# Kernel tuning notes

Hardware: AMD Instinct MI355X
Metric: run time of the kernel (lower is better)

## Reference

```python
import jax, jax.numpy as jnp
import numpy as np

EPS = 1e-7

def squash(t, axis=-1):
    sq = jnp.sum(jnp.square(t), axis=axis, keepdims=True)
    safe_norm = jnp.sqrt(sq + EPS)
    return t * (sq / (1.0 + sq)) / safe_norm


def setup_inputs() -> dict:
    key = jax.random.key(0)
    k1, k2 = jax.random.split(key)
    B, I, Din, N, D = 32, 1024, 32, 64, 32
    x = jax.random.normal(k1, (B, I, Din), dtype=jnp.float32)
    # glorot-ish scale ~ sqrt(2/(Din+D)) = 0.1767; use 0.1
    W = jax.random.normal(k2, (N, I, D, Din), dtype=jnp.float32) * 0.1
    return {"x": x, "W": W, "num_routing": 3}


def _infer(inputs_hat, logits):
    # softmax over the num_capsule axis (axis=1), matching tf.nn.softmax(logits, axis=1)
    route = jax.nn.softmax(logits, axis=1)                      # [B,N,1,I]
    routing = jnp.squeeze(jnp.matmul(route, inputs_hat), -2)    # [B,N,D]
    return squash(routing)


def reference(x, W, num_routing):
    # inputs_hat[b,n,i,d] = sum_k x[b,i,k] * W[n,i,d,k]
    inputs_hat = jnp.einsum('bik,nidk->bnid', x, W)             # [B,N,I,D]
    B, N, I, D = inputs_hat.shape
    ih_stop = jax.lax.stop_gradient(inputs_hat)
    logits = jnp.zeros((B, N, 1, I), dtype=inputs_hat.dtype)
    outputs = None
    for r in range(num_routing):
        if r == num_routing - 1:
            outputs = _infer(inputs_hat, logits)
        else:
            outputs = _infer(ih_stop, logits)
            # distances[b,n,1,i] = <outputs[b,n,:], ih_stop[b,n,i,:]>
            dist = jnp.matmul(outputs[:, :, None, :], jnp.swapaxes(ih_stop, -1, -2))
            logits = logits + dist
    return outputs
```

## Files before the change

### kernel.cpp

```cpp
#include <hip/hip_runtime.h>
#include <stdint.h>

#define II 1024
#define BBc 32
#define NN 64
#define DD 32
#define NDT 2048

typedef _Float16 half8 __attribute__((ext_vector_type(8)));
typedef float f32x4 __attribute__((ext_vector_type(4)));

__device__ __forceinline__ half8 ld_cvt8(const float* __restrict__ p) {
  const float4 v0 = *(const float4*)p;
  const float4 v1 = *(const float4*)(p + 4);
  half8 h;
  h[0] = (_Float16)v0.x; h[1] = (_Float16)v0.y; h[2] = (_Float16)v0.z; h[3] = (_Float16)v0.w;
  h[4] = (_Float16)v1.x; h[5] = (_Float16)v1.y; h[6] = (_Float16)v1.z; h[7] = (_Float16)v1.w;
  return h;
}

__device__ __forceinline__ half8 ld_cvt8_nt(const float* __restrict__ p) {
  const f32x4 v0 = __builtin_nontemporal_load((const f32x4*)p);
  const f32x4 v1 = __builtin_nontemporal_load((const f32x4*)(p + 4));
  half8 h;
  h[0] = (_Float16)v0[0]; h[1] = (_Float16)v0[1]; h[2] = (_Float16)v0[2]; h[3] = (_Float16)v0[3];
  h[4] = (_Float16)v1[0]; h[5] = (_Float16)v1[1]; h[6] = (_Float16)v1[2]; h[7] = (_Float16)v1[3];
  return h;
}

__global__ __launch_bounds__(256) void k1_mfma(
    const float* __restrict__ x, const float* __restrict__ W,
    _Float16* __restrict__ ih)
{
  __shared__ _Float16 lbuf[4][32][64];
  const int t = threadIdx.x;
  const int i = blockIdx.x;
  const int half_ = blockIdx.y;
  const int w = t >> 6;
  const int L = t & 63;
  const int lm = L & 15, q = L >> 4;

  half8 afrag[2];
#pragma unroll
  for (int mt = 0; mt < 2; ++mt)
    afrag[mt] = ld_cvt8(x + ((size_t)(mt * 16 + lm) * II + i) * 32 + q * 8);

  const int ndw = half_ * 1024 + w * 256;
  for (int g = 0; g < 4; ++g) {
#pragma unroll
    for (int nt = 0; nt < 4; ++nt) {
      const int nd = ndw + g * 64 + nt * 16 + lm;
      const int n = nd >> 5, d = nd & 31;
      const half8 bfrag = ld_cvt8_nt(W + (size_t)n * (II * 1024) + (size_t)i * 1024 + d * 32 + q * 8);
      const f32x4 z = {0.f, 0.f, 0.f, 0.f};
      f32x4 acc0 = __builtin_amdgcn_mfma_f32_16x16x32_f16(afrag[0], bfrag, z, 0, 0, 0);
      f32x4 acc1 = __builtin_amdgcn_mfma_f32_16x16x32_f16(afrag[1], bfrag, z, 0, 0, 0);
#pragma unroll
      for (int r = 0; r < 4; ++r) {
        lbuf[w][q * 4 + r][nt * 16 + lm]      = (_Float16)acc0[r];
        lbuf[w][16 + q * 4 + r][nt * 16 + lm] = (_Float16)acc1[r];
      }
    }
    asm volatile("s_waitcnt lgkmcnt(0)" ::: "memory");
    __builtin_amdgcn_sched_barrier(0);
#pragma unroll
    for (int j = 0; j < 4; ++j) {
      const int row = j * 8 + (L >> 3);
      const int ndo = (L & 7) * 8;
      const half8 v = *(const half8*)&lbuf[w][row][ndo];
      *(half8*)(ih + ((size_t)row * II + i) * NDT + ndw + g * 64 + ndo) = v;
    }
    __builtin_amdgcn_sched_barrier(0);
  }
}

__global__ __launch_bounds__(256) void s0red(
    const _Float16* __restrict__ ih, float* __restrict__ s0p)
{
  const int b = blockIdx.x, is = blockIdx.y;
  const int t = threadIdx.x;
  const _Float16* base = ih + ((size_t)b * II + is * 32) * NDT + t * 8;
  float a[8] = {};
#pragma unroll 8
  for (int ii = 0; ii < 32; ++ii) {
    const half8 v = *(const half8*)(base + (size_t)ii * NDT);
#pragma unroll
    for (int j = 0; j < 8; ++j) a[j] += (float)v[j];
  }
  float* o = s0p + ((size_t)is * BBc + b) * NDT + t * 8;
  *(float4*)(o + 0) = make_float4(a[0], a[1], a[2], a[3]);
  *(float4*)(o + 4) = make_float4(a[4], a[5], a[6], a[7]);
}

__global__ __launch_bounds__(256) void k3_route(
    const _Float16* __restrict__ ih, const float* __restrict__ o1,
    const float* __restrict__ o2, float* __restrict__ rpart)
{
  __shared__ float red[4][NN][DD + 1];
  const int t = threadIdx.x;
  const int b = blockIdx.x, it = blockIdx.y;
  const int w = t >> 6, lane = t & 63;
  float outr[DD];
  {
    const float4* p1 = (const float4*)(o1 + ((size_t)b * NN + lane) * DD);
    if (o2 != nullptr) {
      const float4* p2 = (const float4*)(o2 + ((size_t)b * NN + lane) * DD);
#pragma unroll
      for (int qq = 0; qq < 8; ++qq) {
        const float4 v1 = p1[qq], v2 = p2[qq];
        outr[qq * 4 + 0] = v1.x + v2.x; outr[qq * 4 + 1] = v1.y + v2.y;
        outr[qq * 4 + 2] = v1.z + v2.z; outr[qq * 4 + 3] = v1.w + v2.w;
      }
    } else {
#pragma unroll
      for (int qq = 0; qq < 8; ++qq) {
        const float4 v1 = p1[qq];
        outr[qq * 4 + 0] = v1.x; outr[qq * 4 + 1] = v1.y;
        outr[qq * 4 + 2] = v1.z; outr[qq * 4 + 3] = v1.w;
      }
    }
  }
  float racc[DD] = {};
  const _Float16* ibase = ih + (size_t)b * II * NDT + lane * DD;
#pragma unroll
  for (int jj = 0; jj < 4; ++jj) {
    const int i = it * 16 + w * 4 + jj;
    const half8* r8 = (const half8*)(ibase + (size_t)i * NDT);
    float ihr[DD];
#pragma unroll
    for (int qq = 0; qq < 4; ++qq) {
      const half8 v = r8[qq];
#pragma unroll
      for (int j = 0; j < 8; ++j) ihr[qq * 8 + j] = (float)v[j];
    }
    float dist = 0.f;
#pragma unroll
    for (int d = 0; d < DD; ++d) dist += outr[d] * ihr[d];
    float m = dist;
#pragma unroll
    for (int off = 32; off > 0; off >>= 1) m = fmaxf(m, __shfl_xor(m, off));
    const float e = __expf(dist - m);
    float ss = e;
#pragma unroll
    for (int off = 32; off > 0; off >>= 1) ss += __shfl_xor(ss, off);
    const float route = e / ss;
#pragma unroll
    for (int d = 0; d < DD; ++d) racc[d] += route * ihr[d];
  }
#pragma unroll
  for (int d = 0; d < DD; ++d) red[w][lane][d] = racc[d];
  __syncthreads();
  for (int j = t; j < NN * DD; j += 256) {
    const int n = j >> 5, d = j & 31;
    const float v = red[0][n][d] + red[1][n][d] + red[2][n][d] + red[3][n][d];
    rpart[((size_t)it * BBc + b) * NDT + n * DD + d] = v;
  }
}

__global__ __launch_bounds__(256) void k_rs(
    const float* __restrict__ parts, const int nparts, const float scale,
    float* __restrict__ dst)
{
  const int b = blockIdx.x;
  const int ng = blockIdx.y;
  const int t = threadIdx.x;
  const int n = ng * 8 + (t >> 5), d = t & 31;
  const size_t off = (size_t)b * NDT + n * DD + d;
  float s = 0.f;
  for (int c = 0; c < nparts; ++c) s += parts[(size_t)c * (BBc * NDT) + off];
  s *= scale;
  float sq = s * s;
#pragma unroll
  for (int m = 16; m > 0; m >>= 1) sq += __shfl_xor(sq, m);
  const float f = sq / ((1.f + sq) * sqrtf(sq + 1e-7f));
  dst[off] = s * f;
}

extern "C" void kernel_launch(void* const* d_in, const int* in_sizes, int n_in,
                              void* d_out, int out_size, void* d_ws, size_t ws_size,
                              hipStream_t stream) {
  (void)in_sizes; (void)n_in; (void)out_size; (void)ws_size;
  const float* x = (const float*)d_in[0];
  const float* W = (const float*)d_in[1];

  char* ws = (char*)d_ws;
  _Float16* ih = (_Float16*)ws;
  size_t off = (size_t)BBc * II * NDT * 2;
  float* s0p = (float*)(ws + off); off += (size_t)32 * BBc * NDT * 4;
  float* rpart = (float*)(ws + off); off += (size_t)64 * BBc * NDT * 4;
  float* outA = (float*)(ws + off); off += (size_t)BBc * NDT * 4;
  float* outB = (float*)(ws + off);
  float* outF = (float*)d_out;

  k1_mfma<<<dim3(II, 2), 256, 0, stream>>>(x, W, ih);
  s0red<<<dim3(BBc, 32), 256, 0, stream>>>(ih, s0p);
  k_rs<<<dim3(BBc, 8), 256, 0, stream>>>(s0p, 32, 1.f / 64.f, outA);
  k3_route<<<dim3(BBc, 64), 256, 0, stream>>>(ih, outA, nullptr, rpart);
  k_rs<<<dim3(BBc, 8), 256, 0, stream>>>(rpart, 64, 1.f, outB);
  k3_route<<<dim3(BBc, 64), 256, 0, stream>>>(ih, outA, outB, rpart);
  k_rs<<<dim3(BBc, 8), 256, 0, stream>>>(rpart, 64, 1.f, outF);
}
```

Measured before the change: 494.0 us.

## Fuse all capsule routing stages into one cooperative persistent kernel with grid sync

Replaces the seven separate kernel launches with a single cooperative kernel of 1024 blocks that runs every phase in turn and uses grid-wide syncs between them. Each einsum block now handles both halves of the nd range, and each route block handles 32 input capsules instead of 16, which halves the partial-sum buffer and the reduction fan-in. The intent is to remove launch gaps and tail effects between the short routing kernels. In exchange, the einsum phase runs with half as many blocks, grid syncs add their own cost, and the grid only launches cooperatively if 1024 blocks fit resident at once, otherwise the code falls back to separate launches.

```diff
diff --git a/kernel.cpp b/kernel.cpp
--- a/kernel.cpp
+++ b/kernel.cpp
@@ -1,5 +1,8 @@
 #include <hip/hip_runtime.h>
+#include <hip/hip_cooperative_groups.h>
 #include <stdint.h>
+
+namespace cg = cooperative_groups;
 
 #define II 1024
 #define BBc 32
@@ -28,57 +31,52 @@
   return h;
 }
 
-__global__ __launch_bounds__(256) void k1_mfma(
+__device__ __forceinline__ void phase_einsum(
     const float* __restrict__ x, const float* __restrict__ W,
-    _Float16* __restrict__ ih)
-{
-  __shared__ _Float16 lbuf[4][32][64];
-  const int t = threadIdx.x;
-  const int i = blockIdx.x;
-  const int half_ = blockIdx.y;
-  const int w = t >> 6;
-  const int L = t & 63;
-  const int lm = L & 15, q = L >> 4;
-
+    _Float16* __restrict__ ih, _Float16 (*lbuf)[32][64], int bid, int t)
+{
+  const int i = bid;
+  const int w = t >> 6, L = t & 63, lm = L & 15, q = L >> 4;
   half8 afrag[2];
 #pragma unroll
   for (int mt = 0; mt < 2; ++mt)
     afrag[mt] = ld_cvt8(x + ((size_t)(mt * 16 + lm) * II + i) * 32 + q * 8);
 
-  const int ndw = half_ * 1024 + w * 256;
-  for (int g = 0; g < 4; ++g) {
-#pragma unroll
-    for (int nt = 0; nt < 4; ++nt) {
-      const int nd = ndw + g * 64 + nt * 16 + lm;
-      const int n = nd >> 5, d = nd & 31;
-      const half8 bfrag = ld_cvt8_nt(W + (size_t)n * (II * 1024) + (size_t)i * 1024 + d * 32 + q * 8);
-      const f32x4 z = {0.f, 0.f, 0.f, 0.f};
-      f32x4 acc0 = __builtin_amdgcn_mfma_f32_16x16x32_f16(afrag[0], bfrag, z, 0, 0, 0);
-      f32x4 acc1 = __builtin_amdgcn_mfma_f32_16x16x32_f16(afrag[1], bfrag, z, 0, 0, 0);
-#pragma unroll
-      for (int r = 0; r < 4; ++r) {
-        lbuf[w][q * 4 + r][nt * 16 + lm]      = (_Float16)acc0[r];
-        lbuf[w][16 + q * 4 + r][nt * 16 + lm] = (_Float16)acc1[r];
-      }
+  for (int hf = 0; hf < 2; ++hf) {
+    const int ndw = hf * 1024 + w * 256;
+    for (int g = 0; g < 4; ++g) {
+#pragma unroll
+      for (int nt = 0; nt < 4; ++nt) {
+        const int nd = ndw + g * 64 + nt * 16 + lm;
+        const int n = nd >> 5, d = nd & 31;
+        const half8 bfrag = ld_cvt8_nt(W + (size_t)n * (II * 1024) + (size_t)i * 1024 + d * 32 + q * 8);
+        const f32x4 z = {0.f, 0.f, 0.f, 0.f};
+        f32x4 acc0 = __builtin_amdgcn_mfma_f32_16x16x32_f16(afrag[0], bfrag, z, 0, 0, 0);
+        f32x4 acc1 = __builtin_amdgcn_mfma_f32_16x16x32_f16(afrag[1], bfrag, z, 0, 0, 0);
+#pragma unroll
+        for (int r = 0; r < 4; ++r) {
+          lbuf[w][q * 4 + r][nt * 16 + lm]      = (_Float16)acc0[r];
+          lbuf[w][16 + q * 4 + r][nt * 16 + lm] = (_Float16)acc1[r];
+        }
+      }
+      asm volatile("s_waitcnt lgkmcnt(0)" ::: "memory");
+      __builtin_amdgcn_sched_barrier(0);
+#pragma unroll
+      for (int j = 0; j < 4; ++j) {
+        const int row = j * 8 + (L >> 3);
+        const int ndo = (L & 7) * 8;
+        const half8 v = *(const half8*)&lbuf[w][row][ndo];
+        *(half8*)(ih + ((size_t)row * II + i) * NDT + ndw + g * 64 + ndo) = v;
+      }
+      __builtin_amdgcn_sched_barrier(0);
     }
-    asm volatile("s_waitcnt lgkmcnt(0)" ::: "memory");
-    __builtin_amdgcn_sched_barrier(0);
-#pragma unroll
-    for (int j = 0; j < 4; ++j) {
-      const int row = j * 8 + (L >> 3);
-      const int ndo = (L & 7) * 8;
-      const half8 v = *(const half8*)&lbuf[w][row][ndo];
-      *(half8*)(ih + ((size_t)row * II + i) * NDT + ndw + g * 64 + ndo) = v;
-    }
-    __builtin_amdgcn_sched_barrier(0);
-  }
-}
-
-__global__ __launch_bounds__(256) void s0red(
-    const _Float16* __restrict__ ih, float* __restrict__ s0p)
-{
-  const int b = blockIdx.x, is = blockIdx.y;
-  const int t = threadIdx.x;
+  }
+}
+
+__device__ __forceinline__ void phase_s0red(
+    const _Float16* __restrict__ ih, float* __restrict__ s0p, int bid, int t)
+{
+  const int b = bid >> 5, is = bid & 31;
   const _Float16* base = ih + ((size_t)b * II + is * 32) * NDT + t * 8;
   float a[8] = {};
 #pragma unroll 8
@@ -92,13 +90,12 @@
   *(float4*)(o + 4) = make_float4(a[4], a[5], a[6], a[7]);
 }
 
-__global__ __launch_bounds__(256) void k3_route(
+__device__ __forceinline__ void phase_route(
     const _Float16* __restrict__ ih, const float* __restrict__ o1,
-    const float* __restrict__ o2, float* __restrict__ rpart)
-{
-  __shared__ float red[4][NN][DD + 1];
-  const int t = threadIdx.x;
-  const int b = blockIdx.x, it = blockIdx.y;
+    const float* __restrict__ o2, float* __restrict__ rpart,
+    float (*red)[NN][DD + 1], int bid, int t)
+{
+  const int b = bid & 31, it = bid >> 5;
   const int w = t >> 6, lane = t & 63;
   float outr[DD];
   {
@@ -122,20 +119,19 @@
   }
   float racc[DD] = {};
   const _Float16* ibase = ih + (size_t)b * II * NDT + lane * DD;
-#pragma unroll
-  for (int jj = 0; jj < 4; ++jj) {
-    const int i = it * 16 + w * 4 + jj;
+  for (int jj = 0; jj < 8; ++jj) {
+    const int i = it * 32 + w * 8 + jj;
     const half8* r8 = (const half8*)(ibase + (size_t)i * NDT);
-    float ihr[DD];
-#pragma unroll
-    for (int qq = 0; qq < 4; ++qq) {
-      const half8 v = r8[qq];
-#pragma unroll
-      for (int j = 0; j < 8; ++j) ihr[qq * 8 + j] = (float)v[j];
-    }
+    const half8 v0 = r8[0], v1 = r8[1], v2 = r8[2], v3 = r8[3];
     float dist = 0.f;
 #pragma unroll
-    for (int d = 0; d < DD; ++d) dist += outr[d] * ihr[d];
+    for (int j = 0; j < 8; ++j) dist += outr[j]      * (float)v0[j];
+#pragma unroll
+    for (int j = 0; j < 8; ++j) dist += outr[8 + j]  * (float)v1[j];
+#pragma unroll
+    for (int j = 0; j < 8; ++j) dist += outr[16 + j] * (float)v2[j];
+#pragma unroll
+    for (int j = 0; j < 8; ++j) dist += outr[24 + j] * (float)v3[j];
     float m = dist;
 #pragma unroll
     for (int off = 32; off > 0; off >>= 1) m = fmaxf(m, __shfl_xor(m, off));
@@ -145,8 +141,15 @@
     for (int off = 32; off > 0; off >>= 1) ss += __shfl_xor(ss, off);
     const float route = e / ss;
 #pragma unroll
-    for (int d = 0; d < DD; ++d) racc[d] += route * ihr[d];
-  }
+    for (int j = 0; j < 8; ++j) racc[j]      += route * (float)v0[j];
+#pragma unroll
+    for (int j = 0; j < 8; ++j) racc[8 + j]  += route * (float)v1[j];
+#pragma unroll
+    for (int j = 0; j < 8; ++j) racc[16 + j] += route * (float)v2[j];
+#pragma unroll
+    for (int j = 0; j < 8; ++j) racc[24 + j] += route * (float)v3[j];
+  }
+  __syncthreads();
 #pragma unroll
   for (int d = 0; d < DD; ++d) red[w][lane][d] = racc[d];
   __syncthreads();
@@ -157,13 +160,12 @@
   }
 }
 
-__global__ __launch_bounds__(256) void k_rs(
+__device__ __forceinline__ void phase_rs(
     const float* __restrict__ parts, const int nparts, const float scale,
-    float* __restrict__ dst)
-{
-  const int b = blockIdx.x;
-  const int ng = blockIdx.y;
-  const int t = threadIdx.x;
+    float* __restrict__ dst, int bid, int t)
+{
+  if (bid >= 256) return;
+  const int b = bid >> 3, ng = bid & 7;
   const int n = ng * 8 + (t >> 5), d = t & 31;
   const size_t off = (size_t)b * NDT + n * DD + d;
   float s = 0.f;
@@ -176,6 +178,54 @@
   dst[off] = s * f;
 }
 
+__global__ __launch_bounds__(256, 4) void fused_caps(
+    const float* __restrict__ x, const float* __restrict__ W,
+    _Float16* __restrict__ ih, float* __restrict__ s0p, float* __restrict__ rpart,
+    float* __restrict__ outA, float* __restrict__ outB, float* __restrict__ outF)
+{
+  __shared__ union SH {
+    _Float16 lbuf[4][32][64];
+    float    red[4][NN][DD + 1];
+  } sh;
+  cg::grid_group gg = cg::this_grid();
+  const int bid = blockIdx.x, t = threadIdx.x;
+
+  phase_einsum(x, W, ih, sh.lbuf, bid, t);
+  gg.sync();
+  phase_s0red(ih, s0p, bid, t);
+  gg.sync();
+  phase_rs(s0p, 32, 1.f / 64.f, outA, bid, t);
+  gg.sync();
+  phase_route(ih, outA, nullptr, rpart, sh.red, bid, t);
+  gg.sync();
+  phase_rs(rpart, 32, 1.f, outB, bid, t);
+  gg.sync();
+  phase_route(ih, outA, outB, rpart, sh.red, bid, t);
+  gg.sync();
+  phase_rs(rpart, 32, 1.f, outF, bid, t);
+}
+
+__global__ __launch_bounds__(256) void k1_sep(
+    const float* __restrict__ x, const float* __restrict__ W, _Float16* __restrict__ ih) {
+  __shared__ _Float16 lbuf[4][32][64];
+  phase_einsum(x, W, ih, lbuf, blockIdx.x, threadIdx.x);
+}
+__global__ __launch_bounds__(256) void s0_sep(
+    const _Float16* __restrict__ ih, float* __restrict__ s0p) {
+  phase_s0red(ih, s0p, blockIdx.x, threadIdx.x);
+}
+__global__ __launch_bounds__(256) void route_sep(
+    const _Float16* __restrict__ ih, const float* __restrict__ o1,
+    const float* __restrict__ o2, float* __restrict__ rpart) {
+  __shared__ float red[4][NN][DD + 1];
+  phase_route(ih, o1, o2, rpart, red, blockIdx.x, threadIdx.x);
+}
+__global__ __launch_bounds__(256) void rs_sep(
+    const float* __restrict__ parts, const int nparts, const float scale,
+    float* __restrict__ dst) {
+  phase_rs(parts, nparts, scale, dst, blockIdx.x, threadIdx.x);
+}
+
 extern "C" void kernel_launch(void* const* d_in, const int* in_sizes, int n_in,
                               void* d_out, int out_size, void* d_ws, size_t ws_size,
                               hipStream_t stream) {
@@ -187,16 +237,22 @@
   _Float16* ih = (_Float16*)ws;
   size_t off = (size_t)BBc * II * NDT * 2;
   float* s0p = (float*)(ws + off); off += (size_t)32 * BBc * NDT * 4;
-  float* rpart = (float*)(ws + off); off += (size_t)64 * BBc * NDT * 4;
+  float* rpart = (float*)(ws + off); off += (size_t)32 * BBc * NDT * 4;
   float* outA = (float*)(ws + off); off += (size_t)BBc * NDT * 4;
   float* outB = (float*)(ws + off);
   float* outF = (float*)d_out;
 
-  k1_mfma<<<dim3(II, 2), 256, 0, stream>>>(x, W, ih);
-  s0red<<<dim3(BBc, 32), 256, 0, stream>>>(ih, s0p);
-  k_rs<<<dim3(BBc, 8), 256, 0, stream>>>(s0p, 32, 1.f / 64.f, outA);
-  k3_route<<<dim3(BBc, 64), 256, 0, stream>>>(ih, outA, nullptr, rpart);
-  k_rs<<<dim3(BBc, 8), 256, 0, stream>>>(rpart, 64, 1.f, outB);
-  k3_route<<<dim3(BBc, 64), 256, 0, stream>>>(ih, outA, outB, rpart);
-  k_rs<<<dim3(BBc, 8), 256, 0, stream>>>(rpart, 64, 1.f, outF);
-}
+  void* kargs[] = {(void*)&x, (void*)&W, (void*)&ih, (void*)&s0p,
+                   (void*)&rpart, (void*)&outA, (void*)&outB, (void*)&outF};
+  hipError_t rc = hipLaunchCooperativeKernel((const void*)fused_caps,
+                                             dim3(1024), dim3(256), kargs, 0, stream);
+  if (rc != hipSuccess) {
+    k1_sep<<<dim3(1024), 256, 0, stream>>>(x, W, ih);
+    s0_sep<<<dim3(1024), 256, 0, stream>>>(ih, s0p);
+    rs_sep<<<dim3(256), 256, 0, stream>>>(s0p, 32, 1.f / 64.f, outA);
+    route_sep<<<dim3(1024), 256, 0, stream>>>(ih, outA, nullptr, rpart);
+    rs_sep<<<dim3(256), 256, 0, stream>>>(rpart, 32, 1.f, outB);
+    route_sep<<<dim3(1024), 256, 0, stream>>>(ih, outA, outB, rpart);
+    rs_sep<<<dim3(256), 256, 0, stream>>>(rpart, 32, 1.f, outF);
+  }
+}
```

Result: slower. 1.128 ms (+128.3%).
